# Performance work log

Measured on AMD Instinct MI355X. Metric: run time of the kernel, lower is better.

Reference implementation:

```python
import jax, jax.numpy as jnp
import numpy as np

EMBED_DIM = 1024
RANK = 32

def setup_inputs() -> dict:
    key = jax.random.key(0)
    ks = jax.random.split(key, 9)
    B, S, D, R = 4, 4096, EMBED_DIM, RANK
    s_in = 1.0 / np.sqrt(D)
    s_r = 1.0 / np.sqrt(R)
    return {
        "x": jax.random.normal(ks[0], (B, S, D), dtype=jnp.float32),
        # Linear weights stored as [in, out] (transpose of torch layout)
        "Wq": jax.random.uniform(ks[1], (D, R), jnp.float32, -s_in, s_in),
        "bq": jax.random.uniform(ks[2], (R,), jnp.float32, -s_in, s_in),
        "Wk": jax.random.uniform(ks[3], (D, R), jnp.float32, -s_in, s_in),
        "bk": jax.random.uniform(ks[4], (R,), jnp.float32, -s_in, s_in),
        "Wv": jax.random.uniform(ks[5], (D, R), jnp.float32, -s_in, s_in),
        "bv": jax.random.uniform(ks[6], (R,), jnp.float32, -s_in, s_in),
        "Wo": jax.random.uniform(ks[7], (R, D), jnp.float32, -s_r, s_r),
        "bo": jax.random.uniform(ks[8], (D,), jnp.float32, -s_r, s_r),
    }

def reference(x, Wq, bq, Wk, bk, Wv, bv, Wo, bo):
    scale = RANK ** (-0.5)
    Q = jnp.einsum('bsd,dr->bsr', x, Wq) + bq  # [B,S,R]
    K = jnp.einsum('bsd,dr->bsr', x, Wk) + bk
    V = jnp.einsum('bsd,dr->bsr', x, Wv) + bv
    scores = jnp.einsum('bqr,bkr->bqk', Q, K) * scale  # [B,S,S]
    probs = jax.nn.softmax(scores, axis=-1)
    # dropout is identity in eval mode
    attn_out = jnp.einsum('bqk,bkr->bqr', probs, V)  # [B,S,R]
    return jnp.einsum('bsr,rd->bsd', attn_out, Wo) + bo
```

## Files before the change

kernel.cpp:

```cpp
#include <hip/hip_runtime.h>

typedef __bf16 bf16x8 __attribute__((ext_vector_type(8)));
typedef float f32x4 __attribute__((ext_vector_type(4)));

#define MFMA16(a, b, c) __builtin_amdgcn_mfma_f32_16x16x32_bf16((a), (b), (c), 0, 0, 0)

#define WT_OFF   0
#define WOT_OFF  98304
#define QB_OFF   131072
#define KB_OFF   655360
#define VT_OFF   1179648

#define SCALE_R 0.17677669529663689f

__global__ __launch_bounds__(256) void prep_kernel(
    const float* __restrict__ Wq, const float* __restrict__ Wk,
    const float* __restrict__ Wv, const float* __restrict__ Wo,
    __bf16* __restrict__ ws) {
  int idx = blockIdx.x * 256 + threadIdx.x;
  if (idx < 98304) {
    int n = idx >> 10, d = idx & 1023;
    float v;
    if (n < 32)      v = Wq[d * 32 + n] * SCALE_R;
    else if (n < 64) v = Wk[d * 32 + (n - 32)];
    else             v = Wv[d * 32 + (n - 64)];
    ws[WT_OFF + idx] = (__bf16)v;
  } else if (idx < 131072) {
    int j = idx - 98304;
    int d = j >> 5, r = j & 31;
    ws[WOT_OFF + j] = (__bf16)Wo[r * 1024 + d];
  }
}

__global__ __launch_bounds__(256) void proj_kernel(
    const float* __restrict__ x, const float* __restrict__ bq,
    const float* __restrict__ bk, const float* __restrict__ bv,
    __bf16* __restrict__ ws) {
  const __bf16* Wt = ws + WT_OFF;
  __bf16* Qb = ws + QB_OFF;
  __bf16* Kb = ws + KB_OFF;
  __bf16* Vt = ws + VT_OFF;
  int tid = threadIdx.x;
  int lane = tid & 63, w = tid >> 6;
  int c = lane & 15, g = lane >> 4;
  int rowA = blockIdx.x * 64 + w * 16 + c;
  const float* xrow = x + (size_t)rowA * 1024 + g * 8;
  f32x4 acc[6];
#pragma unroll
  for (int i = 0; i < 6; i++) acc[i] = (f32x4){0.f, 0.f, 0.f, 0.f};
#pragma unroll 4
  for (int ks = 0; ks < 32; ks++) {
    float4 xa = *(const float4*)(xrow + ks * 32);
    float4 xb = *(const float4*)(xrow + ks * 32 + 4);
    bf16x8 a;
    a[0] = (__bf16)xa.x; a[1] = (__bf16)xa.y; a[2] = (__bf16)xa.z; a[3] = (__bf16)xa.w;
    a[4] = (__bf16)xb.x; a[5] = (__bf16)xb.y; a[6] = (__bf16)xb.z; a[7] = (__bf16)xb.w;
#pragma unroll
    for (int nf = 0; nf < 6; nf++) {
      bf16x8 b = *(const bf16x8*)(Wt + (nf * 16 + c) * 1024 + ks * 32 + g * 8);
      acc[nf] = MFMA16(a, b, acc[nf]);
    }
  }
  int row0 = blockIdx.x * 64 + w * 16 + g * 4;
#pragma unroll
  for (int nf = 0; nf < 6; nf++) {
    int n = nf * 16 + c;
    float bias = (n < 32) ? bq[n] * SCALE_R : (n < 64 ? bk[n - 32] : bv[n - 64]);
#pragma unroll
    for (int r = 0; r < 4; r++) {
      int row = row0 + r;
      float v = acc[nf][r] + bias;
      if (n < 32)      Qb[row * 32 + n] = (__bf16)v;
      else if (n < 64) Kb[row * 32 + (n - 32)] = (__bf16)v;
      else {
        int batch = row >> 12, s = row & 4095;
        Vt[(batch * 32 + (n - 64)) * 4096 + s] = (__bf16)v;
      }
    }
  }
}

__global__ __launch_bounds__(64) void flash_kernel(
    const float* __restrict__ bo, float* __restrict__ out,
    const __bf16* __restrict__ ws) {
  const __bf16* Wot = ws + WOT_OFF;
  const __bf16* Qb  = ws + QB_OFF;
  const __bf16* Kb  = ws + KB_OFF;
  const __bf16* Vt  = ws + VT_OFF;
  __shared__ __bf16 pbuf[16 * 72];
  __shared__ __bf16 abuf[16 * 40];
  int lane = threadIdx.x;
  int c = lane & 15, g = lane >> 4;
  int batch = blockIdx.x >> 8, qt = blockIdx.x & 255;
  int qrow0 = batch * 4096 + qt * 16;
  const __bf16* Kbb = Kb + (size_t)batch * 4096 * 32;
  const __bf16* Vtb = Vt + (size_t)batch * 32 * 4096;

  const f32x4 zero = {0.f, 0.f, 0.f, 0.f};
  bf16x8 aq = *(const bf16x8*)(Qb + (qrow0 + c) * 32 + g * 8);
  f32x4 acc0 = zero, acc1 = zero;
  float m[4], lsum[4];
#pragma unroll
  for (int r = 0; r < 4; r++) { m[r] = -1e30f; lsum[r] = 0.0f; }

  bf16x8 bk[4], bv[4];
#pragma unroll
  for (int i = 0; i < 4; i++)
    bk[i] = *(const bf16x8*)(Kbb + (i * 16 + c) * 32 + g * 8);
#pragma unroll
  for (int i = 0; i < 4; i++)
    bv[i] = *(const bf16x8*)(Vtb + ((i >> 1) * 16 + c) * 4096 + (i & 1) * 32 + g * 8);

#pragma unroll 2
  for (int kt = 0; kt < 64; kt++) {
    int ktn = (kt + 1 < 64) ? kt + 1 : 63;
    bf16x8 nk[4], nv[4];
#pragma unroll
    for (int i = 0; i < 4; i++)
      nk[i] = *(const bf16x8*)(Kbb + (ktn * 64 + i * 16 + c) * 32 + g * 8);
#pragma unroll
    for (int i = 0; i < 4; i++)
      nv[i] = *(const bf16x8*)(Vtb + ((i >> 1) * 16 + c) * 4096 + ktn * 64 + (i & 1) * 32 + g * 8);

    f32x4 s[4];
#pragma unroll
    for (int i = 0; i < 4; i++) s[i] = MFMA16(aq, bk[i], zero);

    float p[4][4];
#pragma unroll
    for (int r = 0; r < 4; r++) {
      float tmax = fmaxf(fmaxf(s[0][r], s[1][r]), fmaxf(s[2][r], s[3][r]));
#pragma unroll
      for (int msk = 1; msk < 16; msk <<= 1)
        tmax = fmaxf(tmax, __shfl_xor(tmax, msk, 64));
      float mn = fmaxf(m[r], tmax);
      float corr = __expf(m[r] - mn);
      m[r] = mn;
      float ps = 0.0f;
#pragma unroll
      for (int i = 0; i < 4; i++) { p[i][r] = __expf(s[i][r] - mn); ps += p[i][r]; }
#pragma unroll
      for (int msk = 1; msk < 16; msk <<= 1) ps += __shfl_xor(ps, msk, 64);
      lsum[r] = lsum[r] * corr + ps;
      acc0[r] *= corr;
      acc1[r] *= corr;
    }

    __syncthreads();
#pragma unroll
    for (int i = 0; i < 4; i++)
#pragma unroll
      for (int r = 0; r < 4; r++)
        pbuf[(4 * g + r) * 72 + i * 16 + c] = (__bf16)p[i][r];
    __syncthreads();
    bf16x8 ap0 = *(const bf16x8*)(pbuf + c * 72 + g * 8);
    bf16x8 ap1 = *(const bf16x8*)(pbuf + c * 72 + 32 + g * 8);

    acc0 = MFMA16(ap0, bv[0], acc0);
    acc0 = MFMA16(ap1, bv[1], acc0);
    acc1 = MFMA16(ap0, bv[2], acc1);
    acc1 = MFMA16(ap1, bv[3], acc1);

#pragma unroll
    for (int i = 0; i < 4; i++) { bk[i] = nk[i]; bv[i] = nv[i]; }
  }

#pragma unroll
  for (int r = 0; r < 4; r++) {
    float inv = 1.0f / lsum[r];
    acc0[r] *= inv;
    acc1[r] *= inv;
  }
  __syncthreads();
#pragma unroll
  for (int r = 0; r < 4; r++) {
    abuf[(4 * g + r) * 40 + c] = (__bf16)acc0[r];
    abuf[(4 * g + r) * 40 + 16 + c] = (__bf16)acc1[r];
  }
  __syncthreads();
  bf16x8 aa = *(const bf16x8*)(abuf + c * 40 + g * 8);
#pragma unroll 8
  for (int nf = 0; nf < 64; nf++) {
    bf16x8 bw = *(const bf16x8*)(Wot + (nf * 16 + c) * 32 + g * 8);
    f32x4 o = MFMA16(aa, bw, zero);
    float bias = bo[nf * 16 + c];
    float* op = out + (size_t)(qrow0 + 4 * g) * 1024 + nf * 16 + c;
#pragma unroll
    for (int r = 0; r < 4; r++)
      op[(size_t)r * 1024] = o[r] + bias;
  }
}

extern "C" void kernel_launch(void* const* d_in, const int* in_sizes, int n_in,
                              void* d_out, int out_size, void* d_ws, size_t ws_size,
                              hipStream_t stream) {
  const float* x  = (const float*)d_in[0];
  const float* Wq = (const float*)d_in[1];
  const float* bq = (const float*)d_in[2];
  const float* Wk = (const float*)d_in[3];
  const float* bk = (const float*)d_in[4];
  const float* Wv = (const float*)d_in[5];
  const float* bv = (const float*)d_in[6];
  const float* Wo = (const float*)d_in[7];
  const float* bo = (const float*)d_in[8];
  float* out = (float*)d_out;
  __bf16* ws = (__bf16*)d_ws;
  prep_kernel<<<dim3(512), dim3(256), 0, stream>>>(Wq, Wk, Wv, Wo, ws);
  proj_kernel<<<dim3(256), dim3(256), 0, stream>>>(x, bq, bk, bv, ws);
  flash_kernel<<<dim3(1024), dim3(64), 0, stream>>>(bo, out, ws);
}
```

Before: 237.8 us.

## Stage x and K/V tiles in LDS via async global-to-LDS loads, share across waves

Rewrites the projection kernel to run one wave per 16 rows, streaming x tiles into swizzled LDS with global_load_lds and prefetching weight fragments with explicit waitcnt pipelining. The flash kernel now groups four waves per block sharing double-buffered K/V tiles loaded asynchronously into LDS, computes scores transposed so the softmax row reductions need fewer shuffles, and folds log2(e) into the Q scale so it can use exp2f. The aim is less redundant global K/V traffic and shorter softmax reduction chains. The cost is more LDS use and block barriers per tile, plus hand-written waitcnt counts that must match the issued loads exactly.

```diff
diff --git a/kernel.cpp b/kernel.cpp
--- a/kernel.cpp
+++ b/kernel.cpp
@@ -11,7 +11,13 @@
 #define KB_OFF   655360
 #define VT_OFF   1179648
 
-#define SCALE_R 0.17677669529663689f
+#define SCALE_QL (0.17677669529663689f * 1.4426950408889634f)
+
+__device__ __forceinline__ void load_lds16(void* lds, const void* gsrc) {
+  __builtin_amdgcn_global_load_lds(
+      (const __attribute__((address_space(1))) unsigned int*)gsrc,
+      (__attribute__((address_space(3))) unsigned int*)lds, 16, 0, 0);
+}
 
 __global__ __launch_bounds__(256) void prep_kernel(
     const float* __restrict__ Wq, const float* __restrict__ Wk,
@@ -21,7 +27,7 @@
   if (idx < 98304) {
     int n = idx >> 10, d = idx & 1023;
     float v;
-    if (n < 32)      v = Wq[d * 32 + n] * SCALE_R;
+    if (n < 32)      v = Wq[d * 32 + n] * SCALE_QL;
     else if (n < 64) v = Wk[d * 32 + (n - 32)];
     else             v = Wv[d * 32 + (n - 64)];
     ws[WT_OFF + idx] = (__bf16)v;
@@ -32,162 +38,231 @@
   }
 }
 
-__global__ __launch_bounds__(256) void proj_kernel(
+__device__ __forceinline__ void stage_x(float* lbase, const float* x, int r0,
+                                        int tt, int lane) {
+#pragma unroll
+  for (int j = 0; j < 4; ++j) {
+    int row = j * 4 + (lane >> 4);
+    int ch = lane & 15;
+    int gc = (ch & 8) | ((ch & 7) ^ (row & 7));
+    const float* src = x + (size_t)(r0 + row) * 1024 + tt * 64 + gc * 4;
+    load_lds16(lbase + j * 256, src);
+  }
+}
+
+__device__ __forceinline__ void load_w(bf16x8* w, const __bf16* Wt, int t,
+                                       int c, int g) {
+#pragma unroll
+  for (int ks = 0; ks < 2; ++ks)
+#pragma unroll
+    for (int nf = 0; nf < 6; ++nf)
+      w[ks * 6 + nf] =
+          *(const bf16x8*)(Wt + (size_t)(nf * 16 + c) * 1024 + t * 64 + ks * 32 + g * 8);
+}
+
+__global__ __launch_bounds__(64) void proj_kernel(
     const float* __restrict__ x, const float* __restrict__ bq,
     const float* __restrict__ bk, const float* __restrict__ bv,
     __bf16* __restrict__ ws) {
+  __shared__ float xlds[4 * 16 * 64];
   const __bf16* Wt = ws + WT_OFF;
   __bf16* Qb = ws + QB_OFF;
   __bf16* Kb = ws + KB_OFF;
   __bf16* Vt = ws + VT_OFF;
-  int tid = threadIdx.x;
-  int lane = tid & 63, w = tid >> 6;
+  int lane = threadIdx.x;
   int c = lane & 15, g = lane >> 4;
-  int rowA = blockIdx.x * 64 + w * 16 + c;
-  const float* xrow = x + (size_t)rowA * 1024 + g * 8;
+  int r0 = blockIdx.x * 16;
+
+#pragma unroll
+  for (int tt = 0; tt < 4; ++tt) stage_x(xlds + tt * 1024, x, r0, tt, lane);
+  __builtin_amdgcn_sched_barrier(0);
+  bf16x8 wcur[12], wnext[12];
+  load_w(wcur, Wt, 0, c, g);
+  __builtin_amdgcn_sched_barrier(0);
+
   f32x4 acc[6];
 #pragma unroll
-  for (int i = 0; i < 6; i++) acc[i] = (f32x4){0.f, 0.f, 0.f, 0.f};
-#pragma unroll 4
-  for (int ks = 0; ks < 32; ks++) {
-    float4 xa = *(const float4*)(xrow + ks * 32);
-    float4 xb = *(const float4*)(xrow + ks * 32 + 4);
-    bf16x8 a;
-    a[0] = (__bf16)xa.x; a[1] = (__bf16)xa.y; a[2] = (__bf16)xa.z; a[3] = (__bf16)xa.w;
-    a[4] = (__bf16)xb.x; a[5] = (__bf16)xb.y; a[6] = (__bf16)xb.z; a[7] = (__bf16)xb.w;
-#pragma unroll
-    for (int nf = 0; nf < 6; nf++) {
-      bf16x8 b = *(const bf16x8*)(Wt + (nf * 16 + c) * 1024 + ks * 32 + g * 8);
-      acc[nf] = MFMA16(a, b, acc[nf]);
-    }
-  }
-  int row0 = blockIdx.x * 64 + w * 16 + g * 4;
-#pragma unroll
-  for (int nf = 0; nf < 6; nf++) {
+  for (int i = 0; i < 6; ++i) acc[i] = (f32x4){0.f, 0.f, 0.f, 0.f};
+
+  for (int t = 0; t < 16; ++t) {
+    __builtin_amdgcn_sched_barrier(0);
+    if (t + 1 < 16) load_w(wnext, Wt, t + 1, c, g);
+    __builtin_amdgcn_sched_barrier(0);
+    if (t == 0)      asm volatile("s_waitcnt vmcnt(12)" ::: "memory");
+    else if (t < 12) asm volatile("s_waitcnt vmcnt(16)" ::: "memory");
+    else             asm volatile("s_waitcnt vmcnt(0)" ::: "memory");
+    __builtin_amdgcn_sched_barrier(0);
+
+    const float* xt = xlds + (t & 3) * 1024;
+#pragma unroll
+    for (int ks = 0; ks < 2; ++ks) {
+      int cha = (ks << 3) | ((2 * g) ^ (c & 7));
+      int chb = (ks << 3) | (((2 * g) | 1) ^ (c & 7));
+      f32x4 xa = *(const f32x4*)(xt + c * 64 + cha * 4);
+      f32x4 xb = *(const f32x4*)(xt + c * 64 + chb * 4);
+      bf16x8 a;
+      a[0] = (__bf16)xa[0]; a[1] = (__bf16)xa[1];
+      a[2] = (__bf16)xa[2]; a[3] = (__bf16)xa[3];
+      a[4] = (__bf16)xb[0]; a[5] = (__bf16)xb[1];
+      a[6] = (__bf16)xb[2]; a[7] = (__bf16)xb[3];
+#pragma unroll
+      for (int nf = 0; nf < 6; ++nf)
+        acc[nf] = MFMA16(a, wcur[ks * 6 + nf], acc[nf]);
+    }
+    __builtin_amdgcn_sched_barrier(0);
+    if (t + 4 < 16) stage_x(xlds + (t & 3) * 1024, x, r0, t + 4, lane);
+#pragma unroll
+    for (int i = 0; i < 12; ++i) wcur[i] = wnext[i];
+  }
+
+#pragma unroll
+  for (int nf = 0; nf < 6; ++nf) {
     int n = nf * 16 + c;
-    float bias = (n < 32) ? bq[n] * SCALE_R : (n < 64 ? bk[n - 32] : bv[n - 64]);
-#pragma unroll
-    for (int r = 0; r < 4; r++) {
-      int row = row0 + r;
+    float bias = (n < 32) ? bq[n] * SCALE_QL : (n < 64 ? bk[n - 32] : bv[n - 64]);
+#pragma unroll
+    for (int r = 0; r < 4; ++r) {
+      int row = r0 + 4 * g + r;
       float v = acc[nf][r] + bias;
       if (n < 32)      Qb[row * 32 + n] = (__bf16)v;
       else if (n < 64) Kb[row * 32 + (n - 32)] = (__bf16)v;
       else {
         int batch = row >> 12, s = row & 4095;
-        Vt[(batch * 32 + (n - 64)) * 4096 + s] = (__bf16)v;
+        Vt[((size_t)(batch * 32 + (n - 64))) * 4096 + s] = (__bf16)v;
       }
     }
   }
 }
 
-__global__ __launch_bounds__(64) void flash_kernel(
+__device__ __forceinline__ void stage_kv(__bf16* buf, const __bf16* Kbb,
+                                         const __bf16* Vtb, int kt, int w,
+                                         int lane) {
+  if (w < 2) {
+#pragma unroll
+    for (int i = 0; i < 2; ++i) {
+      int row = w * 32 + i * 16 + (lane >> 2);
+      int ch = lane & 3;
+      const __bf16* src = Kbb + (size_t)(kt * 64 + row) * 32 + ch * 8;
+      load_lds16(buf + w * 1024 + i * 512, src);
+    }
+  } else {
+    int t2 = w - 2;
+#pragma unroll
+    for (int i = 0; i < 2; ++i) {
+      int row = t2 * 16 + i * 8 + (lane >> 3);
+      int ch = lane & 7;
+      int gc = ch ^ (row & 7);
+      const __bf16* src = Vtb + (size_t)row * 4096 + kt * 64 + gc * 8;
+      load_lds16(buf + 2048 + t2 * 1024 + i * 512, src);
+    }
+  }
+}
+
+__global__ __launch_bounds__(256) void flash_kernel(
     const float* __restrict__ bo, float* __restrict__ out,
     const __bf16* __restrict__ ws) {
   const __bf16* Wot = ws + WOT_OFF;
   const __bf16* Qb  = ws + QB_OFF;
   const __bf16* Kb  = ws + KB_OFF;
   const __bf16* Vt  = ws + VT_OFF;
-  __shared__ __bf16 pbuf[16 * 72];
-  __shared__ __bf16 abuf[16 * 40];
-  int lane = threadIdx.x;
-  int c = lane & 15, g = lane >> 4;
-  int batch = blockIdx.x >> 8, qt = blockIdx.x & 255;
-  int qrow0 = batch * 4096 + qt * 16;
+  __shared__ __bf16 kv[2][4096];
+  __shared__ __bf16 pbuf[4][16 * 72];
+  __shared__ __bf16 abuf[4][16 * 40];
+  int tid = threadIdx.x;
+  int w = tid >> 6, lane = tid & 63, c = lane & 15, g = lane >> 4;
+  int batch = blockIdx.x >> 6, qb = blockIdx.x & 63;
+  int qrow0 = batch * 4096 + qb * 64 + w * 16;
   const __bf16* Kbb = Kb + (size_t)batch * 4096 * 32;
   const __bf16* Vtb = Vt + (size_t)batch * 32 * 4096;
 
   const f32x4 zero = {0.f, 0.f, 0.f, 0.f};
-  bf16x8 aq = *(const bf16x8*)(Qb + (qrow0 + c) * 32 + g * 8);
+  bf16x8 qfrag = *(const bf16x8*)(Qb + (size_t)(qrow0 + c) * 32 + g * 8);
   f32x4 acc0 = zero, acc1 = zero;
-  float m[4], lsum[4];
-#pragma unroll
-  for (int r = 0; r < 4; r++) { m[r] = -1e30f; lsum[r] = 0.0f; }
-
-  bf16x8 bk[4], bv[4];
-#pragma unroll
-  for (int i = 0; i < 4; i++)
-    bk[i] = *(const bf16x8*)(Kbb + (i * 16 + c) * 32 + g * 8);
-#pragma unroll
-  for (int i = 0; i < 4; i++)
-    bv[i] = *(const bf16x8*)(Vtb + ((i >> 1) * 16 + c) * 4096 + (i & 1) * 32 + g * 8);
-
-#pragma unroll 2
-  for (int kt = 0; kt < 64; kt++) {
-    int ktn = (kt + 1 < 64) ? kt + 1 : 63;
-    bf16x8 nk[4], nv[4];
-#pragma unroll
-    for (int i = 0; i < 4; i++)
-      nk[i] = *(const bf16x8*)(Kbb + (ktn * 64 + i * 16 + c) * 32 + g * 8);
-#pragma unroll
-    for (int i = 0; i < 4; i++)
-      nv[i] = *(const bf16x8*)(Vtb + ((i >> 1) * 16 + c) * 4096 + ktn * 64 + (i & 1) * 32 + g * 8);
-
-    f32x4 s[4];
-#pragma unroll
-    for (int i = 0; i < 4; i++) s[i] = MFMA16(aq, bk[i], zero);
-
+  float m = -1e30f, lsum = 0.f;
+
+  stage_kv(kv[0], Kbb, Vtb, 0, w, lane);
+
+  for (int kt = 0; kt < 64; ++kt) {
+    __syncthreads();
+    if (kt + 1 < 64) stage_kv(kv[(kt + 1) & 1], Kbb, Vtb, kt + 1, w, lane);
+    const __bf16* kvb = kv[kt & 1];
+
+    bf16x8 ak[4], av[4];
+#pragma unroll
+    for (int i = 0; i < 4; ++i)
+      ak[i] = *(const bf16x8*)(kvb + (i * 16 + c) * 32 + g * 8);
+#pragma unroll
+    for (int t2 = 0; t2 < 2; ++t2)
+#pragma unroll
+      for (int ks = 0; ks < 2; ++ks)
+        av[t2 * 2 + ks] = *(const bf16x8*)(kvb + 2048 + (t2 * 16 + c) * 64 +
+                                           (((ks << 2) | g) ^ (c & 7)) * 8);
+
+    f32x4 sr[4];
+#pragma unroll
+    for (int i = 0; i < 4; ++i) sr[i] = MFMA16(ak[i], qfrag, zero);
+
+    float mx = sr[0][0];
+#pragma unroll
+    for (int i = 0; i < 4; ++i)
+#pragma unroll
+      for (int r = 0; r < 4; ++r) mx = fmaxf(mx, sr[i][r]);
+    mx = fmaxf(mx, __shfl_xor(mx, 16, 64));
+    mx = fmaxf(mx, __shfl_xor(mx, 32, 64));
+    float mn = fmaxf(m, mx);
+    float corr = exp2f(m - mn);
+    m = mn;
+    float ps = 0.f;
     float p[4][4];
 #pragma unroll
-    for (int r = 0; r < 4; r++) {
-      float tmax = fmaxf(fmaxf(s[0][r], s[1][r]), fmaxf(s[2][r], s[3][r]));
-#pragma unroll
-      for (int msk = 1; msk < 16; msk <<= 1)
-        tmax = fmaxf(tmax, __shfl_xor(tmax, msk, 64));
-      float mn = fmaxf(m[r], tmax);
-      float corr = __expf(m[r] - mn);
-      m[r] = mn;
-      float ps = 0.0f;
-#pragma unroll
-      for (int i = 0; i < 4; i++) { p[i][r] = __expf(s[i][r] - mn); ps += p[i][r]; }
-#pragma unroll
-      for (int msk = 1; msk < 16; msk <<= 1) ps += __shfl_xor(ps, msk, 64);
-      lsum[r] = lsum[r] * corr + ps;
-      acc0[r] *= corr;
-      acc1[r] *= corr;
-    }
-
-    __syncthreads();
-#pragma unroll
-    for (int i = 0; i < 4; i++)
-#pragma unroll
-      for (int r = 0; r < 4; r++)
-        pbuf[(4 * g + r) * 72 + i * 16 + c] = (__bf16)p[i][r];
-    __syncthreads();
-    bf16x8 ap0 = *(const bf16x8*)(pbuf + c * 72 + g * 8);
-    bf16x8 ap1 = *(const bf16x8*)(pbuf + c * 72 + 32 + g * 8);
-
-    acc0 = MFMA16(ap0, bv[0], acc0);
-    acc0 = MFMA16(ap1, bv[1], acc0);
-    acc1 = MFMA16(ap0, bv[2], acc1);
-    acc1 = MFMA16(ap1, bv[3], acc1);
-
-#pragma unroll
-    for (int i = 0; i < 4; i++) { bk[i] = nk[i]; bv[i] = nv[i]; }
-  }
-
-#pragma unroll
-  for (int r = 0; r < 4; r++) {
-    float inv = 1.0f / lsum[r];
-    acc0[r] *= inv;
-    acc1[r] *= inv;
-  }
-  __syncthreads();
-#pragma unroll
-  for (int r = 0; r < 4; r++) {
-    abuf[(4 * g + r) * 40 + c] = (__bf16)acc0[r];
-    abuf[(4 * g + r) * 40 + 16 + c] = (__bf16)acc1[r];
-  }
-  __syncthreads();
-  bf16x8 aa = *(const bf16x8*)(abuf + c * 40 + g * 8);
-#pragma unroll 8
-  for (int nf = 0; nf < 64; nf++) {
+    for (int i = 0; i < 4; ++i)
+#pragma unroll
+      for (int r = 0; r < 4; ++r) {
+        p[i][r] = exp2f(sr[i][r] - mn);
+        ps += p[i][r];
+      }
+    ps += __shfl_xor(ps, 16, 64);
+    ps += __shfl_xor(ps, 32, 64);
+    lsum = lsum * corr + ps;
+#pragma unroll
+    for (int r = 0; r < 4; ++r) { acc0[r] *= corr; acc1[r] *= corr; }
+
+    __bf16* pw = pbuf[w] + c * 72;
+#pragma unroll
+    for (int i = 0; i < 4; ++i)
+#pragma unroll
+      for (int r = 0; r < 4; ++r)
+        pw[16 * i + 4 * g + r] = (__bf16)p[i][r];
+    asm volatile("s_waitcnt lgkmcnt(0)" ::: "memory");
+    __builtin_amdgcn_sched_barrier(0);
+    bf16x8 pf0 = *(const bf16x8*)(pbuf[w] + c * 72 + g * 8);
+    bf16x8 pf1 = *(const bf16x8*)(pbuf[w] + c * 72 + 32 + g * 8);
+
+    acc0 = MFMA16(av[0], pf0, acc0);
+    acc0 = MFMA16(av[1], pf1, acc0);
+    acc1 = MFMA16(av[2], pf0, acc1);
+    acc1 = MFMA16(av[3], pf1, acc1);
+  }
+
+  float inv = 1.0f / lsum;
+#pragma unroll
+  for (int r = 0; r < 4; ++r) { acc0[r] *= inv; acc1[r] *= inv; }
+  __bf16* aw = abuf[w] + c * 40;
+#pragma unroll
+  for (int r = 0; r < 4; ++r) {
+    aw[4 * g + r] = (__bf16)acc0[r];
+    aw[16 + 4 * g + r] = (__bf16)acc1[r];
+  }
+  asm volatile("s_waitcnt lgkmcnt(0)" ::: "memory");
+  __builtin_amdgcn_sched_barrier(0);
+  bf16x8 aa = *(const bf16x8*)(abuf[w] + c * 40 + g * 8);
+#pragma unroll 4
+  for (int nf = 0; nf < 64; ++nf) {
     bf16x8 bw = *(const bf16x8*)(Wot + (nf * 16 + c) * 32 + g * 8);
     f32x4 o = MFMA16(aa, bw, zero);
     float bias = bo[nf * 16 + c];
     float* op = out + (size_t)(qrow0 + 4 * g) * 1024 + nf * 16 + c;
 #pragma unroll
-    for (int r = 0; r < 4; r++)
-      op[(size_t)r * 1024] = o[r] + bias;
+    for (int r = 0; r < 4; ++r) op[(size_t)r * 1024] = o[r] + bias;
   }
 }
 
@@ -206,6 +281,6 @@
   float* out = (float*)d_out;
   __bf16* ws = (__bf16*)d_ws;
   prep_kernel<<<dim3(512), dim3(256), 0, stream>>>(Wq, Wk, Wv, Wo, ws);
-  proj_kernel<<<dim3(256), dim3(256), 0, stream>>>(x, bq, bk, bv, ws);
-  flash_kernel<<<dim3(1024), dim3(64), 0, stream>>>(bo, out, ws);
-}
+  proj_kernel<<<dim3(1024), dim3(64), 0, stream>>>(x, bq, bk, bv, ws);
+  flash_kernel<<<dim3(256), dim3(256), 0, stream>>>(bo, out, ws);
+}
```

After: 218.4 us. 1.09x faster.
